# Performance work log

Measured on AMD Instinct MI355X. Metric: run time of the kernel, lower is better.

## Reference

```python
import jax, jax.numpy as jnp
import numpy as np

N = 50000      # nodes
E = 800000     # edges (setup guarantees every node appears in col)
IN = 256       # input_size
HID = 64       # hidden_size per head
HEADS = 8      # num_heads
OUT = 40       # output_size
ALPHA = 0.2    # leaky relu slope


def _xavier(k, shape, gain=1.414):
    fan_in, fan_out = shape[-2], shape[-1]
    lim = gain * float(np.sqrt(6.0 / (fan_in + fan_out)))
    return jax.random.uniform(k, shape, jnp.float32, -lim, lim)


def setup_inputs() -> dict:
    key = jax.random.key(0)
    ks = jax.random.split(key, 9)
    x = jax.random.normal(ks[0], (N, IN), jnp.float32)
    row = jax.random.randint(ks[1], (E,), 0, N, jnp.int32)
    # ensure every node id appears in col so torch.unique(col) == arange(N)
    col = jnp.concatenate([
        jax.random.randint(ks[2], (E - N,), 0, N, jnp.int32),
        jnp.arange(N, dtype=jnp.int32),
    ])
    edge_index = jnp.stack([row, col])
    W0 = _xavier(ks[3], (HEADS, IN, HID))
    a0 = _xavier(ks[4], (HEADS, 2 * HID, 1))
    W1 = _xavier(ks[5], (HEADS, HEADS * HID, HID))
    a1 = _xavier(ks[6], (HEADS, 2 * HID, 1))
    Wout = _xavier(ks[7], (HEADS * HID, OUT))
    aout = _xavier(ks[8], (2 * OUT, 1))
    return dict(x=x, edge_index=edge_index, W0=W0, a0=a0, W1=W1, a1=a1,
                Wout=Wout, aout=aout)


def _gat_layer(h, W, a, row, col, concat):
    # h: [N, F_in], W: [F_in, F_out], a: [2*F_out, 1]
    Wh = h @ W                                   # [N, F_out]
    F_out = W.shape[1]
    s_src = (Wh @ a[:F_out]).squeeze(-1)         # [N] Wh1
    s_dst = (Wh @ a[F_out:]).squeeze(-1)         # [N] Wh2
    e = jax.nn.leaky_relu(s_src[row] + s_dst[col], ALPHA)   # [E']
    # per-destination (segment) softmax, numerically stable
    m = jax.ops.segment_max(e, col, num_segments=N)
    ex = jnp.exp(e - m[col])
    denom = jax.ops.segment_sum(ex, col, num_segments=N)
    alpha = ex / denom[col]                      # [E']
    out = jax.ops.segment_sum(Wh[row] * alpha[:, None], col, num_segments=N)
    return jax.nn.elu(out) if concat else out


def reference(x, edge_index, W0, a0, W1, a1, Wout, aout):
    idt = edge_index.dtype
    # module appends unique(col) self-loops; here unique(col) == arange(N)
    row = jnp.concatenate([edge_index[0], jnp.arange(N, dtype=idt)])
    col = jnp.concatenate([edge_index[1], jnp.arange(N, dtype=idt)])
    h = jnp.concatenate(
        [_gat_layer(x, W0[i], a0[i], row, col, True) for i in range(HEADS)], axis=1)
    h = jnp.concatenate(
        [_gat_layer(h, W1[i], a1[i], row, col, True) for i in range(HEADS)], axis=1)
    h = jax.nn.elu(_gat_layer(h, Wout, aout, row, col, False))
    return jax.nn.log_softmax(h, axis=1)
```

## Files before the change

### kernel.cpp

```cpp
#include <hip/hip_runtime.h>
#include <hip/hip_bf16.h>

#define IN_F   256
#define HID    64
#define HEADS  8
#define OUTC   40
#define ALPHA_SLOPE 0.2f
#define F1     (HEADS*HID)

typedef short bf16x8 __attribute__((ext_vector_type(8)));
typedef float f32x4  __attribute__((ext_vector_type(4)));


__global__ void hist_kernel(const int* __restrict__ col, int* __restrict__ cnt,
                            int E, int N) {
    int k = blockIdx.x * 256 + threadIdx.x;
    int tot = E + N;
    if (k >= tot) return;
    int c = (k < E) ? col[k] : (k - E);
    atomicAdd(&cnt[c], 1);
}


__global__ __launch_bounds__(1024) void scan1_kernel(
    const int* __restrict__ cnt, int* __restrict__ excl,
    int* __restrict__ bsum, int N) {
    __shared__ int wsum[16];
    int tid = threadIdx.x;
    int i = blockIdx.x * 1024 + tid;
    int lane = tid & 63, wid = tid >> 6;
    int v = (i < N) ? cnt[i] : 0;
    int incl = v;
    #pragma unroll
    for (int off = 1; off < 64; off <<= 1) {
        int t = __shfl_up(incl, off);
        if (lane >= off) incl += t;
    }
    if (lane == 63) wsum[wid] = incl;
    __syncthreads();
    if (wid == 0) {
        int w = (lane < 16) ? wsum[lane] : 0;
        #pragma unroll
        for (int off = 1; off < 16; off <<= 1) {
            int t = __shfl_up(w, off);
            if (lane >= off) w += t;
        }
        if (lane < 16) wsum[lane] = w;
    }
    __syncthreads();
    int woff = (wid > 0) ? wsum[wid - 1] : 0;
    int e = woff + incl - v;
    if (i < N) excl[i] = e;
    if (tid == 1023) bsum[blockIdx.x] = woff + incl;
}

__global__ void scan2_kernel(const int* __restrict__ bsum, int* __restrict__ boff,
                             int* __restrict__ indptrN, int nb) {
    int lane = threadIdx.x;
    int v = (lane < nb) ? bsum[lane] : 0;
    int incl = v;
    #pragma unroll
    for (int off = 1; off < 64; off <<= 1) {
        int t = __shfl_up(incl, off);
        if (lane >= off) incl += t;
    }
    if (lane < nb) boff[lane] = incl - v;
    if (lane == 63) *indptrN = incl;
}

__global__ void scan3_kernel(const int* __restrict__ boff, int* __restrict__ indptr,
                             int* __restrict__ fill, int N) {
    int i = blockIdx.x * 256 + threadIdx.x;
    if (i >= N) return;
    int e = indptr[i] + boff[i >> 10];
    indptr[i] = e;
    fill[i] = e;
}

__global__ void scatter_kernel(const int* __restrict__ row, const int* __restrict__ col,
                               int* __restrict__ fill, int* __restrict__ csr,
                               int E, int N) {
    int k = blockIdx.x * 256 + threadIdx.x;
    int tot = E + N;
    if (k >= tot) return;
    int c = (k < E) ? col[k] : (k - E);
    int r = (k < E) ? row[k] : (k - E);
    int pos = atomicAdd(&fill[c], 1);
    csr[pos] = r;
}


__global__ void cvt_bf16_kernel(const float* __restrict__ in,
                                __hip_bfloat16* __restrict__ out, long n) {
    long i = ((long)blockIdx.x * 256 + threadIdx.x) * 4;
    if (i + 3 >= n) {
        for (long j = i; j < n; j++) out[j] = __float2bfloat16(in[j]);
        return;
    }
    float4 v = *(const float4*)(in + i);
    out[i + 0] = __float2bfloat16(v.x);
    out[i + 1] = __float2bfloat16(v.y);
    out[i + 2] = __float2bfloat16(v.z);
    out[i + 3] = __float2bfloat16(v.w);
}

__global__ void prep_w8_kernel(const float* __restrict__ W,
                               __hip_bfloat16* __restrict__ Wt, int K) {
    long i = (long)blockIdx.x * 256 + threadIdx.x;
    long tot = (long)HEADS * K * 64;
    if (i >= tot) return;
    int n = i & 63;
    long rest = i >> 6;
    int k = (int)(rest % K);
    int h = (int)(rest / K);
    Wt[((long)h * 64 + n) * K + k] = __float2bfloat16(W[i]);
}

__global__ void prep_wout_kernel(const float* __restrict__ W,
                                 __hip_bfloat16* __restrict__ Wt) {
    int i = blockIdx.x * 256 + threadIdx.x;
    if (i >= 64 * 512) return;
    int k = i & 511;
    int n = i >> 9;
    Wt[i] = __float2bfloat16(n < OUTC ? W[(long)k * OUTC + n] : 0.f);
}


__global__ __launch_bounds__(256) void gemm128(
    const __hip_bfloat16* __restrict__ A, const __hip_bfloat16* __restrict__ Bt,
    __hip_bfloat16* __restrict__ Cb, int M, int K) {
    constexpr int LDA = 40;
    __shared__ __hip_bfloat16 As[128 * LDA];
    __shared__ __hip_bfloat16 Bs[128 * LDA];
    int tid = threadIdx.x;
    int m0 = blockIdx.x * 128;
    int n0 = blockIdx.y * 128;
    int lane = tid & 63, wave = tid >> 6;
    int wm = (wave & 1) * 64, wn = (wave >> 1) * 64;
    int fr = lane & 15, fq = lane >> 4;
    int srow = tid >> 1, scol = (tid & 1) * 16;

    const __hip_bfloat16* Arow = A + (long)min(m0 + srow, M - 1) * K;
    const __hip_bfloat16* Brow = Bt + (long)(n0 + srow) * K;

    f32x4 acc[4][4] = {};

    for (int k0 = 0; k0 < K; k0 += 32) {
        float4 av0 = *(const float4*)(Arow + k0 + scol);
        float4 av1 = *(const float4*)(Arow + k0 + scol + 8);
        float4 bv0 = *(const float4*)(Brow + k0 + scol);
        float4 bv1 = *(const float4*)(Brow + k0 + scol + 8);
        __syncthreads();
        *(float4*)(As + srow * LDA + scol) = av0;
        *(float4*)(As + srow * LDA + scol + 8) = av1;
        *(float4*)(Bs + srow * LDA + scol) = bv0;
        *(float4*)(Bs + srow * LDA + scol + 8) = bv1;
        __syncthreads();
        bf16x8 af[4], bfr[4];
        #pragma unroll
        for (int mi = 0; mi < 4; mi++)
            af[mi] = *(const bf16x8*)(As + (wm + mi * 16 + fr) * LDA + fq * 8);
        #pragma unroll
        for (int ni = 0; ni < 4; ni++)
            bfr[ni] = *(const bf16x8*)(Bs + (wn + ni * 16 + fr) * LDA + fq * 8);
        #pragma unroll
        for (int mi = 0; mi < 4; mi++)
            #pragma unroll
            for (int ni = 0; ni < 4; ni++)
                acc[mi][ni] = __builtin_amdgcn_mfma_f32_16x16x32_bf16(
                    af[mi], bfr[ni], acc[mi][ni], 0, 0, 0);
    }

    #pragma unroll
    for (int mi = 0; mi < 4; mi++)
        #pragma unroll
        for (int ni = 0; ni < 4; ni++)
            #pragma unroll
            for (int rr = 0; rr < 4; rr++) {
                int m = m0 + wm + mi * 16 + fq * 4 + rr;
                int n = n0 + wn + ni * 16 + fr;
                if (m < M)
                    Cb[(long)m * F1 + n] = __float2bfloat16(acc[mi][ni][rr]);
            }
}


__global__ __launch_bounds__(256) void gemm_mfma(
    const __hip_bfloat16* __restrict__ A, const __hip_bfloat16* __restrict__ Bt,
    float* __restrict__ C, int M, int K, int NcolsTot) {
    constexpr int LDA = 40;
    __shared__ __hip_bfloat16 As[128 * LDA];
    __shared__ __hip_bfloat16 Bs[64 * LDA];
    int tid = threadIdx.x;
    int m0 = blockIdx.x * 128;
    int lane = tid & 63, wave = tid >> 6;
    int wm = wave * 32;
    int arow = tid >> 2, acol = (tid & 3) * 8;
    int fr = lane & 15, fq = lane >> 4;

    f32x4 acc[2][4] = {};

    for (int k0 = 0; k0 < K; k0 += 32) {
        int ma = min(m0 + arow, M - 1);
        int mb = min(m0 + 64 + arow, M - 1);
        float4 av1 = *(const float4*)(A + (long)ma * K + k0 + acol);
        float4 av2 = *(const float4*)(A + (long)mb * K + k0 + acol);
        float4 bv  = *(const float4*)(Bt + (long)arow * K + k0 + acol);
        __syncthreads();
        *(float4*)(As + arow * LDA + acol) = av1;
        *(float4*)(As + (64 + arow) * LDA + acol) = av2;
        *(float4*)(Bs + arow * LDA + acol) = bv;
        __syncthreads();
        bf16x8 a0 = *(const bf16x8*)(As + (wm + fr) * LDA + fq * 8);
        bf16x8 a1 = *(const bf16x8*)(As + (wm + 16 + fr) * LDA + fq * 8);
        #pragma unroll
        for (int ni = 0; ni < 4; ni++) {
            bf16x8 b = *(const bf16x8*)(Bs + (ni * 16 + fr) * LDA + fq * 8);
            acc[0][ni] = __builtin_amdgcn_mfma_f32_16x16x32_bf16(a0, b, acc[0][ni], 0, 0, 0);
            acc[1][ni] = __builtin_amdgcn_mfma_f32_16x16x32_bf16(a1, b, acc[1][ni], 0, 0, 0);
        }
    }

    #pragma unroll
    for (int mi = 0; mi < 2; mi++)
        #pragma unroll
        for (int ni = 0; ni < 4; ni++)
            #pragma unroll
            for (int rr = 0; rr < 4; rr++) {
                int m = m0 + wm + mi * 16 + fq * 4 + rr;
                int n = ni * 16 + fr;
                if (m < M && n < NcolsTot)
                    C[(long)m * NcolsTot + n] = acc[mi][ni][rr];
            }
}


__global__ __launch_bounds__(256) void scores8_kernel(
    const __hip_bfloat16* __restrict__ Whb, const float* __restrict__ a,
    float* __restrict__ ssrc, float* __restrict__ sdst, int N) {
    int wid = blockIdx.x * 4 + (threadIdx.x >> 6);
    if (wid >= N * HEADS) return;
    int node = wid >> 3, head = wid & 7, lane = threadIdx.x & 63;
    float w = __bfloat162float(Whb[(long)node * F1 + head * HID + lane]);
    float ss = w * a[head * 2 * HID + lane];
    float sd = w * a[head * 2 * HID + HID + lane];
    #pragma unroll
    for (int o = 32; o; o >>= 1) {
        ss += __shfl_xor(ss, o);
        sd += __shfl_xor(sd, o);
    }
    if (lane == 0) {
        ssrc[node * HEADS + head] = ss;
        sdst[node * HEADS + head] = sd;
    }
}

__global__ __launch_bounds__(256) void scores1_kernel(
    const float* __restrict__ Wh, const float* __restrict__ a,
    float* __restrict__ ssrc, float* __restrict__ sdst, int N) {
    int node = blockIdx.x * 4 + (threadIdx.x >> 6);
    if (node >= N) return;
    int lane = threadIdx.x & 63;
    float w = (lane < OUTC) ? Wh[(long)node * OUTC + lane] : 0.f;
    float ss = (lane < OUTC) ? w * a[lane] : 0.f;
    float sd = (lane < OUTC) ? w * a[OUTC + lane] : 0.f;
    #pragma unroll
    for (int o = 32; o; o >>= 1) {
        ss += __shfl_xor(ss, o);
        sd += __shfl_xor(sd, o);
    }
    if (lane == 0) {
        ssrc[node] = ss;
        sdst[node] = sd;
    }
}


__global__ __launch_bounds__(256) void agg8_kernel(
    const __hip_bfloat16* __restrict__ Whb, const float* __restrict__ ssrc,
    const float* __restrict__ sdst, const int* __restrict__ csr,
    const int* __restrict__ indptr, __hip_bfloat16* __restrict__ H, int N) {
    int node = blockIdx.x * 4 + (threadIdx.x >> 6);
    if (node >= N) return;
    int lane = threadIdx.x & 63;
    int h = lane >> 3;
    int e8 = lane & 7;
    int base_h = lane & 56;
    int s = __builtin_amdgcn_readfirstlane(indptr[node]);
    int e = __builtin_amdgcn_readfirstlane(indptr[node + 1]);
    float sd = sdst[node * HEADS + h];

    float acc[8] = {};
    float m_run = -1e30f, d_run = 0.f;

    for (int jb = s; jb < e; jb += 8) {
        int cnt = min(8, e - jb);
        int src_i = 0;
        float x_i = -1e30f;
        if (e8 < cnt) {
            src_i = csr[jb + e8];
            float x = ssrc[src_i * HEADS + h] + sd;
            x_i = x > 0.f ? x : ALPHA_SLOPE * x;
        }
        float tm = x_i;
        tm = fmaxf(tm, __shfl_xor(tm, 1));
        tm = fmaxf(tm, __shfl_xor(tm, 2));
        tm = fmaxf(tm, __shfl_xor(tm, 4));
        float nm = fmaxf(m_run, tm);
        float scale = __expf(m_run - nm);
        #pragma unroll
        for (int k = 0; k < 8; k++) acc[k] *= scale;
        d_run *= scale;
        m_run = nm;
        float w_i = __expf(x_i - nm);
        float ts = w_i;
        ts += __shfl_xor(ts, 1);
        ts += __shfl_xor(ts, 2);
        ts += __shfl_xor(ts, 4);
        d_run += ts;
        for (int u = 0; u < cnt; u++) {
            float wj = __shfl(w_i, base_h + u);
            int   su = __shfl(src_i, u);
            const uint4* rp = (const uint4*)(Whb + (long)su * F1 + lane * 8);
            uint4 d = *rp;
            acc[0] += wj * __uint_as_float(d.x << 16);
            acc[1] += wj * __uint_as_float(d.x & 0xffff0000u);
            acc[2] += wj * __uint_as_float(d.y << 16);
            acc[3] += wj * __uint_as_float(d.y & 0xffff0000u);
            acc[4] += wj * __uint_as_float(d.z << 16);
            acc[5] += wj * __uint_as_float(d.z & 0xffff0000u);
            acc[6] += wj * __uint_as_float(d.w << 16);
            acc[7] += wj * __uint_as_float(d.w & 0xffff0000u);
        }
    }

    float inv = 1.f / d_run;
    unsigned short us[8];
    #pragma unroll
    for (int k = 0; k < 8; k++) {
        float v = acc[k] * inv;
        v = v > 0.f ? v : (__expf(v) - 1.f);
        __hip_bfloat16 b = __float2bfloat16(v);
        __builtin_memcpy(&us[k], &b, 2);
    }
    uint4 ov;
    __builtin_memcpy(&ov, us, 16);
    *(uint4*)(H + (long)node * F1 + lane * 8) = ov;
}

__global__ __launch_bounds__(256) void aggout_kernel(
    const float* __restrict__ Wh, const float* __restrict__ ssrc,
    const float* __restrict__ sdst, const int* __restrict__ csr,
    const int* __restrict__ indptr, float* __restrict__ out, int N) {
    int node = blockIdx.x * 4 + (threadIdx.x >> 6);
    if (node >= N) return;
    int lane = threadIdx.x & 63;
    int s = __builtin_amdgcn_readfirstlane(indptr[node]);
    int e = __builtin_amdgcn_readfirstlane(indptr[node + 1]);
    float sd = sdst[node];
    int lc = min(lane, OUTC - 1);
    const float* whb = Wh + lc;

    float m_run = -1e30f, d_run = 0.f, acc = 0.f;
    for (int t = s; t < e; t += 64) {
        int cnt = min(64, e - t);
        int src_i = node;
        float x_i = -1e30f;
        if (lane < cnt) {
            src_i = csr[t + lane];
            float x = ssrc[src_i] + sd;
            x_i = x > 0.f ? x : ALPHA_SLOPE * x;
        }
        float tm = x_i;
        #pragma unroll
        for (int o = 32; o; o >>= 1) tm = fmaxf(tm, __shfl_xor(tm, o));
        float nm = fmaxf(m_run, tm);
        float scale = __expf(m_run - nm);
        acc *= scale; d_run *= scale;
        m_run = nm;
        float w_i = __expf(x_i - nm);
        float ts = w_i;
        #pragma unroll
        for (int o = 32; o; o >>= 1) ts += __shfl_xor(ts, o);
        d_run += ts;
        int cnt4 = (cnt + 3) & ~3;
        for (int j = 0; j < cnt4; j += 4) {
            #pragma unroll
            for (int u = 0; u < 4; u++) {
                int   sj = __shfl(src_i, j + u);
                float wj = __shfl(w_i,  j + u);
                acc += wj * whb[(long)sj * OUTC];
            }
        }
    }
    float g = acc / d_run;
    float v = g > 0.f ? g : (__expf(g) - 1.f);
    float vm = (lane < OUTC) ? v : -1e30f;
    #pragma unroll
    for (int o = 32; o; o >>= 1) vm = fmaxf(vm, __shfl_xor(vm, o));
    float ex = (lane < OUTC) ? __expf(v - vm) : 0.f;
    #pragma unroll
    for (int o = 32; o; o >>= 1) ex += __shfl_xor(ex, o);
    if (lane < OUTC) out[(long)node * OUTC + lane] = v - vm - logf(ex);
}


extern "C" void kernel_launch(void* const* d_in, const int* in_sizes, int n_in,
                              void* d_out, int out_size, void* d_ws, size_t ws_size,
                              hipStream_t stream) {
    const float* x    = (const float*)d_in[0];
    const int*   ei   = (const int*)d_in[1];
    const float* W0   = (const float*)d_in[2];
    const float* a0   = (const float*)d_in[3];
    const float* W1   = (const float*)d_in[4];
    const float* a1   = (const float*)d_in[5];
    const float* Wout = (const float*)d_in[6];
    const float* aout = (const float*)d_in[7];
    float* out = (float*)d_out;

    const int N = in_sizes[0] / IN_F;
    const int E = in_sizes[1] / 2;
    const int Etot = E + N;
    const int* erow = ei;
    const int* ecol = ei + E;

    char* p = (char*)d_ws;
    auto carve = [&](size_t bytes) {
        void* r = (void*)p;
        p += (bytes + 255) & ~(size_t)255;
        return r;
    };
    float*           Wh   = (float*)carve((size_t)N * OUTC * 4);
    __hip_bfloat16*  Whb  = (__hip_bfloat16*)carve((size_t)N * F1 * 2);
    __hip_bfloat16*  Hb   = (__hip_bfloat16*)carve((size_t)N * F1 * 2);
    __hip_bfloat16*  xb   = (__hip_bfloat16*)carve((size_t)N * IN_F * 2);
    __hip_bfloat16*  Wt0  = (__hip_bfloat16*)carve((size_t)F1 * IN_F * 2);
    __hip_bfloat16*  Wt1  = (__hip_bfloat16*)carve((size_t)F1 * F1 * 2);
    __hip_bfloat16*  WtO  = (__hip_bfloat16*)carve((size_t)64 * F1 * 2);
    float*  ssrc   = (float*)carve((size_t)N * HEADS * 4);
    float*  sdst   = (float*)carve((size_t)N * HEADS * 4);
    int*    cnt    = (int*)carve((size_t)N * 4);
    int*    indptr = (int*)carve((size_t)(N + 1) * 4);
    int*    fill   = (int*)carve((size_t)N * 4);
    int*    csr    = (int*)carve((size_t)Etot * 4);
    int*    bsum   = (int*)carve(64 * 4);
    int*    boff   = (int*)carve(64 * 4);

    hipMemsetAsync(cnt, 0, (size_t)N * 4, stream);
    int eb = (Etot + 255) / 256;
    int nb = (N + 1023) / 1024;
    hist_kernel<<<eb, 256, 0, stream>>>(ecol, cnt, E, N);
    scan1_kernel<<<nb, 1024, 0, stream>>>(cnt, indptr, bsum, N);
    scan2_kernel<<<1, 64, 0, stream>>>(bsum, boff, indptr + N, nb);
    scan3_kernel<<<(N + 255) / 256, 256, 0, stream>>>(boff, indptr, fill, N);
    scatter_kernel<<<eb, 256, 0, stream>>>(erow, ecol, fill, csr, E, N);

    long nx = (long)N * IN_F;
    cvt_bf16_kernel<<<(int)((nx / 4 + 255) / 256), 256, 0, stream>>>(x, xb, nx);
    prep_w8_kernel<<<(HEADS * IN_F * 64 + 255) / 256, 256, 0, stream>>>(W0, Wt0, IN_F);
    prep_w8_kernel<<<(HEADS * F1 * 64 + 255) / 256, 256, 0, stream>>>(W1, Wt1, F1);
    prep_wout_kernel<<<(64 * 512 + 255) / 256, 256, 0, stream>>>(Wout, WtO);

    int mt128 = (N + 127) / 128;
    int wb8 = (N * HEADS + 3) / 4;
    int wb1 = (N + 3) / 4;

    gemm128<<<dim3(mt128, 4), 256, 0, stream>>>(xb, Wt0, Whb, N, IN_F);
    scores8_kernel<<<wb8, 256, 0, stream>>>(Whb, a0, ssrc, sdst, N);
    agg8_kernel<<<wb1, 256, 0, stream>>>(Whb, ssrc, sdst, csr, indptr, Hb, N);

    gemm128<<<dim3(mt128, 4), 256, 0, stream>>>(Hb, Wt1, Whb, N, F1);
    scores8_kernel<<<wb8, 256, 0, stream>>>(Whb, a1, ssrc, sdst, N);
    agg8_kernel<<<wb1, 256, 0, stream>>>(Whb, ssrc, sdst, csr, indptr, Hb, N);

    gemm_mfma<<<dim3(mt128, 1), 256, 0, stream>>>(Hb, WtO, Wh, N, F1, OUTC);
    scores1_kernel<<<wb1, 256, 0, stream>>>(Wh, aout, ssrc, sdst, N);
    aggout_kernel<<<wb1, 256, 0, stream>>>(Wh, ssrc, sdst, csr, indptr, out, N);
}
```

Before: 726.4 us.

## Fuse attention score computation into GEMM epilogues and batch aggregation gathers

Computes the per-head source and destination attention scores inside the GEMM epilogues from fp32 accumulators, using cross-lane reductions, and removes the separate score kernels along with their re-read of Wh. The output layer's projected features are now stored as bf16, halving gather traffic in the final aggregation. The aggregation loop issues all eight row gathers before accumulating when a full group is present, which raises memory-level parallelism. The costs are extra shuffles in the GEMM epilogue, more registers, and slightly lower precision in the output aggregation.

```diff
diff --git a/kernel.cpp b/kernel.cpp
--- a/kernel.cpp
+++ b/kernel.cpp
@@ -20,7 +20,6 @@
     int c = (k < E) ? col[k] : (k - E);
     atomicAdd(&cnt[c], 1);
 }
-
 
 __global__ __launch_bounds__(1024) void scan1_kernel(
     const int* __restrict__ cnt, int* __restrict__ excl,
@@ -128,7 +127,8 @@
 
 __global__ __launch_bounds__(256) void gemm128(
     const __hip_bfloat16* __restrict__ A, const __hip_bfloat16* __restrict__ Bt,
-    __hip_bfloat16* __restrict__ Cb, int M, int K) {
+    __hip_bfloat16* __restrict__ Cb, const float* __restrict__ av,
+    float* __restrict__ ssrc, float* __restrict__ sdst, int M, int K) {
     constexpr int LDA = 40;
     __shared__ __hip_bfloat16 As[128 * LDA];
     __shared__ __hip_bfloat16 Bs[128 * LDA];
@@ -139,6 +139,7 @@
     int wm = (wave & 1) * 64, wn = (wave >> 1) * 64;
     int fr = lane & 15, fq = lane >> 4;
     int srow = tid >> 1, scol = (tid & 1) * 16;
+    int h = blockIdx.y * 2 + (wave >> 1);
 
     const __hip_bfloat16* Arow = A + (long)min(m0 + srow, M - 1) * K;
     const __hip_bfloat16* Brow = Bt + (long)(n0 + srow) * K;
@@ -182,12 +183,42 @@
                 if (m < M)
                     Cb[(long)m * F1 + n] = __float2bfloat16(acc[mi][ni][rr]);
             }
-}
-
-
-__global__ __launch_bounds__(256) void gemm_mfma(
+
+    const float* ah = av + h * 2 * HID;
+    float a_src[4], a_dst[4];
+    #pragma unroll
+    for (int ni = 0; ni < 4; ni++) {
+        a_src[ni] = ah[ni * 16 + fr];
+        a_dst[ni] = ah[64 + ni * 16 + fr];
+    }
+    #pragma unroll
+    for (int mi = 0; mi < 4; mi++)
+        #pragma unroll
+        for (int rr = 0; rr < 4; rr++) {
+            float ps = 0.f, pd = 0.f;
+            #pragma unroll
+            for (int ni = 0; ni < 4; ni++) {
+                ps += acc[mi][ni][rr] * a_src[ni];
+                pd += acc[mi][ni][rr] * a_dst[ni];
+            }
+            #pragma unroll
+            for (int o = 1; o < 16; o <<= 1) {
+                ps += __shfl_xor(ps, o);
+                pd += __shfl_xor(pd, o);
+            }
+            int m = m0 + wm + mi * 16 + fq * 4 + rr;
+            if (fr == 0 && m < M) {
+                ssrc[m * HEADS + h] = ps;
+                sdst[m * HEADS + h] = pd;
+            }
+        }
+}
+
+
+__global__ __launch_bounds__(256) void gemm_out(
     const __hip_bfloat16* __restrict__ A, const __hip_bfloat16* __restrict__ Bt,
-    float* __restrict__ C, int M, int K, int NcolsTot) {
+    __hip_bfloat16* __restrict__ Cb, const float* __restrict__ av,
+    float* __restrict__ ssrc, float* __restrict__ sdst, int M, int K) {
     constexpr int LDA = 40;
     __shared__ __hip_bfloat16 As[128 * LDA];
     __shared__ __hip_bfloat16 Bs[64 * LDA];
@@ -229,50 +260,38 @@
             for (int rr = 0; rr < 4; rr++) {
                 int m = m0 + wm + mi * 16 + fq * 4 + rr;
                 int n = ni * 16 + fr;
-                if (m < M && n < NcolsTot)
-                    C[(long)m * NcolsTot + n] = acc[mi][ni][rr];
-            }
-}
-
-
-__global__ __launch_bounds__(256) void scores8_kernel(
-    const __hip_bfloat16* __restrict__ Whb, const float* __restrict__ a,
-    float* __restrict__ ssrc, float* __restrict__ sdst, int N) {
-    int wid = blockIdx.x * 4 + (threadIdx.x >> 6);
-    if (wid >= N * HEADS) return;
-    int node = wid >> 3, head = wid & 7, lane = threadIdx.x & 63;
-    float w = __bfloat162float(Whb[(long)node * F1 + head * HID + lane]);
-    float ss = w * a[head * 2 * HID + lane];
-    float sd = w * a[head * 2 * HID + HID + lane];
-    #pragma unroll
-    for (int o = 32; o; o >>= 1) {
-        ss += __shfl_xor(ss, o);
-        sd += __shfl_xor(sd, o);
-    }
-    if (lane == 0) {
-        ssrc[node * HEADS + head] = ss;
-        sdst[node * HEADS + head] = sd;
-    }
-}
-
-__global__ __launch_bounds__(256) void scores1_kernel(
-    const float* __restrict__ Wh, const float* __restrict__ a,
-    float* __restrict__ ssrc, float* __restrict__ sdst, int N) {
-    int node = blockIdx.x * 4 + (threadIdx.x >> 6);
-    if (node >= N) return;
-    int lane = threadIdx.x & 63;
-    float w = (lane < OUTC) ? Wh[(long)node * OUTC + lane] : 0.f;
-    float ss = (lane < OUTC) ? w * a[lane] : 0.f;
-    float sd = (lane < OUTC) ? w * a[OUTC + lane] : 0.f;
-    #pragma unroll
-    for (int o = 32; o; o >>= 1) {
-        ss += __shfl_xor(ss, o);
-        sd += __shfl_xor(sd, o);
-    }
-    if (lane == 0) {
-        ssrc[node] = ss;
-        sdst[node] = sd;
-    }
+                if (m < M && n < OUTC)
+                    Cb[(long)m * OUTC + n] = __float2bfloat16(acc[mi][ni][rr]);
+            }
+
+    float a_src[4], a_dst[4];
+    #pragma unroll
+    for (int ni = 0; ni < 4; ni++) {
+        int c = ni * 16 + fr;
+        a_src[ni] = (c < OUTC) ? av[c] : 0.f;
+        a_dst[ni] = (c < OUTC) ? av[OUTC + c] : 0.f;
+    }
+    #pragma unroll
+    for (int mi = 0; mi < 2; mi++)
+        #pragma unroll
+        for (int rr = 0; rr < 4; rr++) {
+            float ps = 0.f, pd = 0.f;
+            #pragma unroll
+            for (int ni = 0; ni < 4; ni++) {
+                ps += acc[mi][ni][rr] * a_src[ni];
+                pd += acc[mi][ni][rr] * a_dst[ni];
+            }
+            #pragma unroll
+            for (int o = 1; o < 16; o <<= 1) {
+                ps += __shfl_xor(ps, o);
+                pd += __shfl_xor(pd, o);
+            }
+            int m = m0 + wm + mi * 16 + fq * 4 + rr;
+            if (fr == 0 && m < M) {
+                ssrc[m] = ps;
+                sdst[m] = pd;
+            }
+        }
 }
 
 
@@ -289,6 +308,7 @@
     int s = __builtin_amdgcn_readfirstlane(indptr[node]);
     int e = __builtin_amdgcn_readfirstlane(indptr[node + 1]);
     float sd = sdst[node * HEADS + h];
+    const __hip_bfloat16* wl = Whb + lane * 8;
 
     float acc[8] = {};
     float m_run = -1e30f, d_run = 0.f;
@@ -318,19 +338,40 @@
         ts += __shfl_xor(ts, 2);
         ts += __shfl_xor(ts, 4);
         d_run += ts;
-        for (int u = 0; u < cnt; u++) {
-            float wj = __shfl(w_i, base_h + u);
-            int   su = __shfl(src_i, u);
-            const uint4* rp = (const uint4*)(Whb + (long)su * F1 + lane * 8);
-            uint4 d = *rp;
-            acc[0] += wj * __uint_as_float(d.x << 16);
-            acc[1] += wj * __uint_as_float(d.x & 0xffff0000u);
-            acc[2] += wj * __uint_as_float(d.y << 16);
-            acc[3] += wj * __uint_as_float(d.y & 0xffff0000u);
-            acc[4] += wj * __uint_as_float(d.z << 16);
-            acc[5] += wj * __uint_as_float(d.z & 0xffff0000u);
-            acc[6] += wj * __uint_as_float(d.w << 16);
-            acc[7] += wj * __uint_as_float(d.w & 0xffff0000u);
+
+        if (cnt == 8) {
+            uint4 d[8];
+            #pragma unroll
+            for (int u = 0; u < 8; u++) {
+                int su = __shfl(src_i, u);
+                d[u] = *(const uint4*)(wl + (long)su * F1);
+            }
+            #pragma unroll
+            for (int u = 0; u < 8; u++) {
+                float wj = __shfl(w_i, base_h + u);
+                acc[0] += wj * __uint_as_float(d[u].x << 16);
+                acc[1] += wj * __uint_as_float(d[u].x & 0xffff0000u);
+                acc[2] += wj * __uint_as_float(d[u].y << 16);
+                acc[3] += wj * __uint_as_float(d[u].y & 0xffff0000u);
+                acc[4] += wj * __uint_as_float(d[u].z << 16);
+                acc[5] += wj * __uint_as_float(d[u].z & 0xffff0000u);
+                acc[6] += wj * __uint_as_float(d[u].w << 16);
+                acc[7] += wj * __uint_as_float(d[u].w & 0xffff0000u);
+            }
+        } else {
+            for (int u = 0; u < cnt; u++) {
+                float wj = __shfl(w_i, base_h + u);
+                int   su = __shfl(src_i, u);
+                uint4 d = *(const uint4*)(wl + (long)su * F1);
+                acc[0] += wj * __uint_as_float(d.x << 16);
+                acc[1] += wj * __uint_as_float(d.x & 0xffff0000u);
+                acc[2] += wj * __uint_as_float(d.y << 16);
+                acc[3] += wj * __uint_as_float(d.y & 0xffff0000u);
+                acc[4] += wj * __uint_as_float(d.z << 16);
+                acc[5] += wj * __uint_as_float(d.z & 0xffff0000u);
+                acc[6] += wj * __uint_as_float(d.w << 16);
+                acc[7] += wj * __uint_as_float(d.w & 0xffff0000u);
+            }
         }
     }
 
@@ -348,8 +389,9 @@
     *(uint4*)(H + (long)node * F1 + lane * 8) = ov;
 }
 
+
 __global__ __launch_bounds__(256) void aggout_kernel(
-    const float* __restrict__ Wh, const float* __restrict__ ssrc,
+    const __hip_bfloat16* __restrict__ Whb, const float* __restrict__ ssrc,
     const float* __restrict__ sdst, const int* __restrict__ csr,
     const int* __restrict__ indptr, float* __restrict__ out, int N) {
     int node = blockIdx.x * 4 + (threadIdx.x >> 6);
@@ -359,7 +401,7 @@
     int e = __builtin_amdgcn_readfirstlane(indptr[node + 1]);
     float sd = sdst[node];
     int lc = min(lane, OUTC - 1);
-    const float* whb = Wh + lc;
+    const __hip_bfloat16* whb = Whb + lc;
 
     float m_run = -1e30f, d_run = 0.f, acc = 0.f;
     for (int t = s; t < e; t += 64) {
@@ -389,7 +431,7 @@
             for (int u = 0; u < 4; u++) {
                 int   sj = __shfl(src_i, j + u);
                 float wj = __shfl(w_i,  j + u);
-                acc += wj * whb[(long)sj * OUTC];
+                acc += wj * __bfloat162float(whb[(long)sj * OUTC]);
             }
         }
     }
@@ -430,9 +472,9 @@
         p += (bytes + 255) & ~(size_t)255;
         return r;
     };
-    float*           Wh   = (float*)carve((size_t)N * OUTC * 4);
     __hip_bfloat16*  Whb  = (__hip_bfloat16*)carve((size_t)N * F1 * 2);
     __hip_bfloat16*  Hb   = (__hip_bfloat16*)carve((size_t)N * F1 * 2);
+    __hip_bfloat16*  WhOb = (__hip_bfloat16*)carve((size_t)N * OUTC * 2);
     __hip_bfloat16*  xb   = (__hip_bfloat16*)carve((size_t)N * IN_F * 2);
     __hip_bfloat16*  Wt0  = (__hip_bfloat16*)carve((size_t)F1 * IN_F * 2);
     __hip_bfloat16*  Wt1  = (__hip_bfloat16*)carve((size_t)F1 * F1 * 2);
@@ -462,18 +504,14 @@
     prep_wout_kernel<<<(64 * 512 + 255) / 256, 256, 0, stream>>>(Wout, WtO);
 
     int mt128 = (N + 127) / 128;
-    int wb8 = (N * HEADS + 3) / 4;
     int wb1 = (N + 3) / 4;
 
-    gemm128<<<dim3(mt128, 4), 256, 0, stream>>>(xb, Wt0, Whb, N, IN_F);
-    scores8_kernel<<<wb8, 256, 0, stream>>>(Whb, a0, ssrc, sdst, N);
+    gemm128<<<dim3(mt128, 4), 256, 0, stream>>>(xb, Wt0, Whb, a0, ssrc, sdst, N, IN_F);
     agg8_kernel<<<wb1, 256, 0, stream>>>(Whb, ssrc, sdst, csr, indptr, Hb, N);
 
-    gemm128<<<dim3(mt128, 4), 256, 0, stream>>>(Hb, Wt1, Whb, N, F1);
-    scores8_kernel<<<wb8, 256, 0, stream>>>(Whb, a1, ssrc, sdst, N);
+    gemm128<<<dim3(mt128, 4), 256, 0, stream>>>(Hb, Wt1, Whb, a1, ssrc, sdst, N, F1);
     agg8_kernel<<<wb1, 256, 0, stream>>>(Whb, ssrc, sdst, csr, indptr, Hb, N);
 
-    gemm_mfma<<<dim3(mt128, 1), 256, 0, stream>>>(Hb, WtO, Wh, N, F1, OUTC);
-    scores1_kernel<<<wb1, 256, 0, stream>>>(Wh, aout, ssrc, sdst, N);
-    aggout_kernel<<<wb1, 256, 0, stream>>>(Wh, ssrc, sdst, csr, indptr, out, N);
-}
+    gemm_out<<<dim3(mt128, 1), 256, 0, stream>>>(Hb, WtO, WhOb, aout, ssrc, sdst, N, F1);
+    aggout_kernel<<<wb1, 256, 0, stream>>>(WhOb, ssrc, sdst, csr, indptr, out, N);
+}
```

Measured after the change: 623.7 us. 1.16x faster.
